# Kernel tuning notes

Measured on AMD Instinct MI355X. Metric: run time of the kernel, lower is better.

The kernel has to match this reference:

```python
import jax, jax.numpy as jnp
import numpy as np

B, C, H, W = 16, 128, 64, 64
NH = 8
HD = C // NH          # head dim == pos_embed_dim
WIN = 5               # relative-position window
OUT = 512             # out_dim of the final 1x1 projection


def _dwconv(x, w, pad):
    """Depthwise 2D conv, x: (N, Cin, H, W), w: (Cin, 1, kh, kw)."""
    return jax.lax.conv_general_dilated(
        x, w, window_strides=(1, 1), padding=[(pad, pad), (pad, pad)],
        dimension_numbers=('NCHW', 'OIHW', 'NCHW'),
        feature_group_count=x.shape[1])


def setup_inputs() -> dict:
    key = jax.random.key(0)
    ks = jax.random.split(key, 6)
    src = jax.random.normal(ks[0], (B, C, H, W), jnp.float32)
    cpe_w = jax.random.normal(ks[1], (C, 1, 3, 3), jnp.float32) * 0.1
    qkv_w = jax.random.normal(ks[2], (3 * C, C), jnp.float32) * (1.0 / np.sqrt(C))
    rel_pos = jax.random.normal(ks[3], (HD, WIN, WIN), jnp.float32) * 0.02
    conv1d_w = jax.random.normal(ks[4], (3,), jnp.float32) * 0.5
    out_w = jax.random.normal(ks[5], (OUT, 2 * C), jnp.float32) * (1.0 / np.sqrt(2 * C))
    return dict(src=src, cpe_w=cpe_w, qkv_w=qkv_w, rel_pos=rel_pos,
                conv1d_w=conv1d_w, out_w=out_w)


def reference(src, cpe_w, qkv_w, rel_pos, conv1d_w, out_w):
    scaling = HD ** (-0.5)
    feature_raw = src

    # CPE: depthwise 3x3 conv residual
    s = _dwconv(src, cpe_w, 1) + src

    # 1x1 QKV conv == channel GEMM
    qkv = jnp.einsum('oc,bchw->bohw', qkv_w, s)          # (B, 3C, H, W)
    q, k, v = jnp.split(qkv, 3, axis=1)                  # each (B, C, H, W)

    q = q.reshape(B * NH, HD, H, W)
    k = k.reshape(B * NH, HD, H, W)
    v = v.reshape(B * NH, HD, H, W)

    N = H * W
    kf = jax.nn.softmax(k.reshape(B * NH, HD, N), axis=-1)   # softmax over spatial
    vf = v.reshape(B * NH, HD, N)
    content_lambda = jnp.einsum('bin,bon->bio', kf, vf)      # (B*NH, HD, HD)
    qf = q.reshape(B * NH, HD, N) * scaling
    content_output = jnp.einsum('bin,bio->bon', qf, content_lambda)
    content_output = content_output.reshape(B * NH, HD, H, W)

    # relative-position lambda: depthwise 5x5 conv of v with rel_pos_embed
    position_lambda = _dwconv(v, rel_pos[:, None, :, :], WIN // 2)
    position_output = q * position_lambda

    result1 = (content_output + position_output).reshape(B, C, H, W)

    # ECA-style channel attention on the raw input
    pool = jnp.mean(feature_raw, axis=(2, 3))                # (B, C)
    xp = jnp.pad(pool, ((0, 0), (1, 1)))
    ca = jax.nn.sigmoid(conv1d_w[0] * xp[:, :-2]
                        + conv1d_w[1] * xp[:, 1:-1]
                        + conv1d_w[2] * xp[:, 2:])           # (B, C)
    result2 = feature_raw * ca[:, :, None, None]

    cat = jnp.concatenate([result1, result2], axis=1)       # (B, 2C, H, W)
    return jnp.einsum('oc,bchw->bohw', out_w, cat)           # (B, OUT, H, W)
```

## Files before the change

kernel.cpp:

```cpp
#include <hip/hip_runtime.h>
#include <hip/hip_bf16.h>
#include <math.h>

#define Bb   16
#define Cc   128
#define Hh   64
#define Wwid 64
#define Nn   4096
#define NHh  8
#define HDd  16
#define BHh  128
#define TCc  384
#define OUTc 512
#define KK2  256

typedef _Float16 f16x8 __attribute__((ext_vector_type(8)));
typedef float    f32x4 __attribute__((ext_vector_type(4)));

__device__ __forceinline__ ushort f2h_bits(float f) {
    _Float16 h = (_Float16)f;
    ushort u;
    __builtin_memcpy(&u, &h, 2);
    return u;
}
__device__ __forceinline__ float h2f_bits(ushort u) {
    _Float16 h;
    __builtin_memcpy(&h, &u, 2);
    return (float)h;
}

__global__ void cvt_weights(const float* __restrict__ a, int na,
                            const float* __restrict__ b2, int nb,
                            ushort* __restrict__ ya, ushort* __restrict__ yb) {
    int i = blockIdx.x * 256 + threadIdx.x;
    if (i < na) ya[i] = f2h_bits(a[i]);
    else if (i < na + nb) yb[i - na] = f2h_bits(b2[i - na]);
}

__global__ void __launch_bounds__(256) cpe_pool_kernel(const float* __restrict__ src,
                                                       const float* __restrict__ cpe_w,
                                                       ushort* __restrict__ s,
                                                       float* __restrict__ pool) {
    int bc = blockIdx.x;
    int c  = bc & (Cc - 1);
    const float* sp = src + (size_t)bc * Nn;
    __shared__ float pl[66 * 66];
    __shared__ float red[256];
    int t = threadIdx.x;
    for (int i = t; i < 66 * 66; i += 256) pl[i] = 0.f;
    __syncthreads();
    float lsum = 0.f;
    for (int i = t; i < Nn / 4; i += 256) {
        float4 v4 = ((const float4*)sp)[i];
        lsum += v4.x + v4.y + v4.z + v4.w;
        int e = i * 4, y = e >> 6, x = e & 63;
        float* d = &pl[(y + 1) * 66 + x + 1];
        d[0] = v4.x; d[1] = v4.y; d[2] = v4.z; d[3] = v4.w;
    }
    red[t] = lsum;
    float w[9];
#pragma unroll
    for (int k = 0; k < 9; k++) w[k] = cpe_w[c * 9 + k];
    __syncthreads();
    for (int s2 = 128; s2 > 0; s2 >>= 1) {
        if (t < s2) red[t] += red[t + s2];
        __syncthreads();
    }
    if (t == 0) pool[bc] = red[0] * (1.0f / Nn);
    int x = t & 63, ys = (t >> 6) * 16;
    float r[3][3];
#pragma unroll
    for (int k = 0; k < 2; k++)
#pragma unroll
        for (int j = 0; j < 3; j++) r[k][j] = pl[(ys + k) * 66 + x + j];
    ushort* dst = s + (size_t)bc * Nn;
#pragma unroll
    for (int yy = 0; yy < 16; yy++) {
        int y = ys + yy;
#pragma unroll
        for (int j = 0; j < 3; j++) r[2][j] = pl[(y + 2) * 66 + x + j];
        float acc = r[1][1];
#pragma unroll
        for (int k = 0; k < 3; k++)
#pragma unroll
            for (int j = 0; j < 3; j++) acc += r[k][j] * w[k * 3 + j];
        dst[y * 64 + x] = f2h_bits(acc);
#pragma unroll
        for (int j = 0; j < 3; j++) { r[0][j] = r[1][j]; r[1][j] = r[2][j]; }
    }
}

__global__ void ca_kernel(const float* __restrict__ pool,
                          const float* __restrict__ w3,
                          float* __restrict__ ca) {
    int i = blockIdx.x * 256 + threadIdx.x;
    if (i >= Bb * Cc) return;
    int c = i & (Cc - 1);
    float left  = (c == 0)        ? 0.f : pool[i - 1];
    float mid   = pool[i];
    float right = (c == Cc - 1)   ? 0.f : pool[i + 1];
    float v = w3[0] * left + w3[1] * mid + w3[2] * right;
    ca[i] = 1.f / (1.f + expf(-v));
}

__global__ void transpose_s(const ushort* __restrict__ s, ushort* __restrict__ sT) {
    int bz = blockIdx.z;
    int c0 = blockIdx.y * 64;
    int n0 = blockIdx.x * 64;
    __shared__ ushort t[64][68];
    int nn = threadIdx.x & 63, c4 = threadIdx.x >> 6;
    const ushort* sp = s + ((size_t)bz * Cc + c0) * Nn + n0;
#pragma unroll
    for (int p = 0; p < 16; p++) {
        int cc = p * 4 + c4;
        t[cc][nn] = sp[(size_t)cc * Nn + nn];
    }
    __syncthreads();
    int cw = threadIdx.x & 63, n4 = threadIdx.x >> 6;
    ushort* dp = sT + ((size_t)bz * Nn + n0) * Cc + c0;
#pragma unroll
    for (int p = 0; p < 16; p++) {
        int n = p * 4 + n4;
        dp[(size_t)n * Cc + cw] = t[cw][n];
    }
}

template<int K, int M, int MODE>
__global__ void __launch_bounds__(256) gemm_tn(const ushort* __restrict__ A,
                                               const ushort* __restrict__ Bt,
                                               float* __restrict__ C,
                                               ushort* __restrict__ q16,
                                               float* __restrict__ kf32,
                                               ushort* __restrict__ v16) {
    const int bz = blockIdx.z;
    const int m0 = blockIdx.y * 128;
    const int n0 = blockIdx.x * 128;
    __shared__ __align__(16) ushort Al[128 * 32];
    __shared__ __align__(16) ushort Bl[128 * 32];
    const int tid  = threadIdx.x;
    const int wave = tid >> 6, lane = tid & 63;
    const int r = lane & 15, q = lane >> 4;
    const int wr = wave >> 1, wc = wave & 1;

    const ushort* Ag = A + (size_t)m0 * K;
    const ushort* Bg = Bt + ((size_t)bz * Nn + n0) * K;

    f32x4 acc[4][4] = {};

    for (int k0 = 0; k0 < K; k0 += 32) {
#pragma unroll
        for (int p = 0; p < 2; p++) {
            int seg = p * 4 + wave;
            int idx = seg * 64 + lane;
            int row = idx >> 2, ch = idx & 3;
            const ushort* ga = Ag + (size_t)row * K + k0 + ch * 8;
            const ushort* gb = Bg + (size_t)row * K + k0 + ch * 8;
            __builtin_amdgcn_global_load_lds(
                (const __attribute__((address_space(1))) void*)(const void*)ga,
                (__attribute__((address_space(3))) void*)(void*)(Al + seg * 512),
                16, 0, 0);
            __builtin_amdgcn_global_load_lds(
                (const __attribute__((address_space(1))) void*)(const void*)gb,
                (__attribute__((address_space(3))) void*)(void*)(Bl + seg * 512),
                16, 0, 0);
        }
        __syncthreads();

        const ushort* Apt = Al + (size_t)(wr * 64 + r) * 32 + q * 8;
        const ushort* Bpt = Bl + (size_t)(wc * 64 + r) * 32 + q * 8;
        f16x8 af[4], bf[4];
#pragma unroll
        for (int i = 0; i < 4; i++) af[i] = *(const f16x8*)(Apt + i * 16 * 32);
#pragma unroll
        for (int j = 0; j < 4; j++) bf[j] = *(const f16x8*)(Bpt + j * 16 * 32);
#pragma unroll
        for (int i = 0; i < 4; i++)
#pragma unroll
            for (int j = 0; j < 4; j++)
                acc[i][j] = __builtin_amdgcn_mfma_f32_16x16x32_f16(af[i], bf[j], acc[i][j], 0, 0, 0);
        __syncthreads();
    }

    if constexpr (MODE == 0) {
        float* Cp = C + ((size_t)bz * M + m0 + wr * 64) * Nn + n0 + wc * 64;
#pragma unroll
        for (int i = 0; i < 4; i++)
#pragma unroll
            for (int j = 0; j < 4; j++)
#pragma unroll
                for (int e = 0; e < 4; e++)
                    Cp[(size_t)(i * 16 + q * 4 + e) * Nn + j * 16 + r] = acc[i][j][e];
    } else {
        size_t base = ((size_t)bz * Cc + wr * 64) * Nn + n0 + wc * 64;
        if (blockIdx.y == 1) {
            float* Cp = kf32 + base;
#pragma unroll
            for (int i = 0; i < 4; i++)
#pragma unroll
                for (int j = 0; j < 4; j++)
#pragma unroll
                    for (int e = 0; e < 4; e++)
                        Cp[(size_t)(i * 16 + q * 4 + e) * Nn + j * 16 + r] = acc[i][j][e];
        } else {
            ushort* Cp = (blockIdx.y == 0 ? q16 : v16) + base;
#pragma unroll
            for (int i = 0; i < 4; i++)
#pragma unroll
                for (int j = 0; j < 4; j++)
#pragma unroll
                    for (int e = 0; e < 4; e++)
                        Cp[(size_t)(i * 16 + q * 4 + e) * Nn + j * 16 + r] = f2h_bits(acc[i][j][e]);
        }
    }
}

__global__ void krowstat(const float* __restrict__ kf32,
                         float* __restrict__ mx, float* __restrict__ irs) {
    int row = blockIdx.x;
    const float* p = kf32 + (size_t)row * Nn;
    int t = threadIdx.x;
    __shared__ float red[256];
    float m = -1e30f;
    float vals[16];
#pragma unroll
    for (int j = 0; j < 16; j++) {
        vals[j] = p[t + j * 256];
        m = fmaxf(m, vals[j]);
    }
    red[t] = m; __syncthreads();
    for (int s2 = 128; s2 > 0; s2 >>= 1) {
        if (t < s2) red[t] = fmaxf(red[t], red[t + s2]);
        __syncthreads();
    }
    m = red[0]; __syncthreads();
    float sum = 0.f;
#pragma unroll
    for (int j = 0; j < 16; j++) sum += __expf(vals[j] - m);
    red[t] = sum; __syncthreads();
    for (int s2 = 128; s2 > 0; s2 >>= 1) {
        if (t < s2) red[t] += red[t + s2];
        __syncthreads();
    }
    if (t == 0) { mx[row] = m; irs[row] = 1.f / red[0]; }
}

__global__ void __launch_bounds__(256) lambda_mfma(const float* __restrict__ kf32,
                                                   const ushort* __restrict__ v16,
                                                   const float* __restrict__ mx,
                                                   const float* __restrict__ irs,
                                                   float* __restrict__ lamP) {
    int bh   = blockIdx.x >> 1;
    int half = blockIdx.x & 1;
    int b = bh >> 3, h = bh & 7;
    int wave = threadIdx.x >> 6, lane = threadIdx.x & 63;
    int r = lane & 15, q = lane >> 4;
    const float*  kf = kf32 + ((size_t)b * Cc + h * HDd) * Nn;
    const ushort* vf = v16  + ((size_t)b * Cc + h * HDd) * Nn;
    float mrow = mx[b * Cc + h * HDd + r];

    f32x4 acc = {};
    int nbase = half * 2048 + wave * 512;
#pragma unroll 4
    for (int s = 0; s < 16; s++) {
        int n = nbase + s * 32 + q * 8;
        float4 ka = *(const float4*)(kf + (size_t)r * Nn + n);
        float4 kb = *(const float4*)(kf + (size_t)r * Nn + n + 4);
        f16x8 bf = *(const f16x8*)(vf + (size_t)r * Nn + n);
        f16x8 af;
        af[0] = (_Float16)__expf(ka.x - mrow);
        af[1] = (_Float16)__expf(ka.y - mrow);
        af[2] = (_Float16)__expf(ka.z - mrow);
        af[3] = (_Float16)__expf(ka.w - mrow);
        af[4] = (_Float16)__expf(kb.x - mrow);
        af[5] = (_Float16)__expf(kb.y - mrow);
        af[6] = (_Float16)__expf(kb.z - mrow);
        af[7] = (_Float16)__expf(kb.w - mrow);
        acc = __builtin_amdgcn_mfma_f32_16x16x32_f16(af, bf, acc, 0, 0, 0);
    }

    __shared__ float red[4][256];
#pragma unroll
    for (int e = 0; e < 4; e++) red[wave][lane * 4 + e] = acc[e];
    __syncthreads();
    if (wave == 0) {
#pragma unroll
        for (int e = 0; e < 4; e++) {
            float v = red[0][lane * 4 + e] + red[1][lane * 4 + e]
                    + red[2][lane * 4 + e] + red[3][lane * 4 + e];
            int row = q * 4 + e;
            v *= irs[b * Cc + h * HDd + row];
            lamP[(size_t)half * (BHh * 256) + bh * 256 + row * 16 + r] = v;
        }
    }
}

__global__ void __launch_bounds__(256) poslam_kernel(const ushort* __restrict__ v16,
                                                     const float* __restrict__ rel,
                                                     ushort* __restrict__ pos) {
    int bc = blockIdx.x;
    int c = bc & (Cc - 1);
    const ushort* vp = v16 + (size_t)bc * Nn;
    __shared__ float pl[68 * 68];
    int t = threadIdx.x;
    for (int i = t; i < 68 * 68; i += 256) pl[i] = 0.f;
    __syncthreads();
    for (int i = t; i < Nn / 8; i += 256) {
        uint4 u = ((const uint4*)vp)[i];
        ushort us[8]; *(uint4*)us = u;
        int e = i * 8, y = e >> 6, x = e & 63;
        float* d = &pl[(y + 2) * 68 + x + 2];
#pragma unroll
        for (int j = 0; j < 8; j++) d[j] = h2f_bits(us[j]);
    }
    float w[25];
#pragma unroll
    for (int k = 0; k < 25; k++) w[k] = rel[(c & (HDd - 1)) * 25 + k];
    __syncthreads();
    int x = t & 63, ys = (t >> 6) * 16;
    float r[5][5];
#pragma unroll
    for (int k = 0; k < 4; k++)
#pragma unroll
        for (int j = 0; j < 5; j++) r[k][j] = pl[(ys + k) * 68 + x + j];
    ushort* dst = pos + (size_t)bc * Nn;
#pragma unroll
    for (int yy = 0; yy < 16; yy++) {
        int y = ys + yy;
#pragma unroll
        for (int j = 0; j < 5; j++) r[4][j] = pl[(y + 4) * 68 + x + j];
        float acc = 0.f;
#pragma unroll
        for (int k = 0; k < 5; k++)
#pragma unroll
            for (int j = 0; j < 5; j++) acc += r[k][j] * w[k * 5 + j];
        dst[y * 64 + x] = f2h_bits(acc);
#pragma unroll
        for (int k = 0; k < 4; k++)
#pragma unroll
            for (int j = 0; j < 5; j++) r[k][j] = r[k + 1][j];
    }
}

__global__ void combine_kernel(const ushort* __restrict__ q16,
                               const float* __restrict__ lamP,
                               const ushort* __restrict__ pos,
                               ushort* __restrict__ catT) {
    int bh   = blockIdx.x >> 4;
    int tile = blockIdx.x & 15;
    int n = tile * 256 + threadIdx.x;
    int b = bh >> 3, h = bh & 7;
    __shared__ float lam_s[256];
    lam_s[threadIdx.x] = lamP[bh * 256 + threadIdx.x]
                       + lamP[(size_t)(BHh * 256) + bh * 256 + threadIdx.x];
    __syncthreads();
    const ushort* qp = q16 + ((size_t)b * Cc + h * HDd) * Nn;
    float qv[16];
#pragma unroll
    for (int i = 0; i < 16; i++) qv[i] = h2f_bits(qp[(size_t)i * Nn + n]);
    const ushort* pp = pos + ((size_t)b * Cc + h * HDd) * Nn;
    float vals[16];
#pragma unroll
    for (int o = 0; o < 16; o++) {
        float co = 0.f;
#pragma unroll
        for (int i2 = 0; i2 < 16; i2++) co += qv[i2] * lam_s[i2 * 16 + o];
        vals[o] = co * 0.25f + qv[o] * h2f_bits(pp[(size_t)o * Nn + n]);
    }
    uint up[8];
#pragma unroll
    for (int o2 = 0; o2 < 8; o2++)
        up[o2] = (uint)f2h_bits(vals[2 * o2]) | ((uint)f2h_bits(vals[2 * o2 + 1]) << 16);
    uint4* dst = (uint4*)(catT + ((size_t)b * Nn + n) * KK2 + h * HDd);
    dst[0] = make_uint4(up[0], up[1], up[2], up[3]);
    dst[1] = make_uint4(up[4], up[5], up[6], up[7]);
}

__global__ void eca_cat(const float* __restrict__ src, const float* __restrict__ ca,
                        ushort* __restrict__ catT) {
    int bz = blockIdx.z, c0 = blockIdx.y * 64, n0 = blockIdx.x * 64;
    __shared__ ushort t[64][68];
    int nn = threadIdx.x & 63, c4 = threadIdx.x >> 6;
    const float* sp  = src + ((size_t)bz * Cc + c0) * Nn + n0;
    const float* cap = ca + bz * Cc + c0;
#pragma unroll
    for (int p = 0; p < 16; p++) {
        int cc = p * 4 + c4;
        t[cc][nn] = f2h_bits(sp[(size_t)cc * Nn + nn] * cap[cc]);
    }
    __syncthreads();
    int cw = threadIdx.x & 63, n4 = threadIdx.x >> 6;
    ushort* dp = catT + ((size_t)bz * Nn + n0) * KK2 + Cc + c0;
#pragma unroll
    for (int p = 0; p < 16; p++) {
        int n = p * 4 + n4;
        dp[(size_t)n * KK2 + cw] = t[cw][n];
    }
}

extern "C" void kernel_launch(void* const* d_in, const int* in_sizes, int n_in,
                              void* d_out, int out_size, void* d_ws, size_t ws_size,
                              hipStream_t stream) {
    const float* src      = (const float*)d_in[0];
    const float* cpe_w    = (const float*)d_in[1];
    const float* qkv_w    = (const float*)d_in[2];
    const float* rel_pos  = (const float*)d_in[3];
    const float* conv1d_w = (const float*)d_in[4];
    const float* out_w    = (const float*)d_in[5];
    float* out = (float*)d_out;

    char* ws = (char*)d_ws;
    ushort* q16   = (ushort*)ws;                                 ws += (size_t)Bb * Cc * Nn * 2;
    float*  kf32  = (float*)ws;                                  ws += (size_t)Bb * Cc * Nn * 4;
    ushort* v16   = (ushort*)ws;                                 ws += (size_t)Bb * Cc * Nn * 2;
    ushort* pos   = (ushort*)ws;                                 ws += (size_t)Bb * Cc * Nn * 2;
    ushort* catT  = (ushort*)ws;                                 ws += (size_t)Bb * Nn * KK2 * 2;
    ushort* sT    = (ushort*)ws;                                 ws += (size_t)Bb * Nn * Cc * 2;
    ushort* s16   = (ushort*)catT;
    float*  lamP  = (float*)ws;                                  ws += (size_t)2 * BHh * HDd * HDd * 4;
    float*  pool  = (float*)ws;                                  ws += Bb * Cc * 4;
    float*  ca    = (float*)ws;                                  ws += Bb * Cc * 4;
    float*  mx    = (float*)ws;                                  ws += Bb * Cc * 4;
    float*  irs   = (float*)ws;                                  ws += Bb * Cc * 4;
    ushort* wq16  = (ushort*)ws;                                 ws += (size_t)TCc * Cc * 2;
    ushort* wo16  = (ushort*)ws;                                 ws += (size_t)OUTc * KK2 * 2;

    {
        int na = TCc * Cc, nb = OUTc * KK2;
        cvt_weights<<<(na + nb + 255) / 256, 256, 0, stream>>>(qkv_w, na, out_w, nb, wq16, wo16);
    }
    cpe_pool_kernel<<<Bb * Cc, 256, 0, stream>>>(src, cpe_w, s16, pool);
    ca_kernel<<<(Bb * Cc + 255) / 256, 256, 0, stream>>>(pool, conv1d_w, ca);
    {
        dim3 g(Nn / 64, Cc / 64, Bb);
        transpose_s<<<g, 256, 0, stream>>>(s16, sT);
    }
    {
        dim3 g(Nn / 128, TCc / 128, Bb);
        gemm_tn<Cc, TCc, 1><<<g, 256, 0, stream>>>(wq16, sT, nullptr, q16, kf32, v16);
    }
    krowstat<<<Bb * Cc, 256, 0, stream>>>(kf32, mx, irs);
    lambda_mfma<<<2 * BHh, 256, 0, stream>>>(kf32, v16, mx, irs, lamP);
    poslam_kernel<<<Bb * Cc, 256, 0, stream>>>(v16, rel_pos, pos);
    combine_kernel<<<BHh * (Nn / 256), 256, 0, stream>>>(q16, lamP, pos, catT);
    {
        dim3 g(Nn / 64, Cc / 64, Bb);
        eca_cat<<<g, 256, 0, stream>>>(src, ca, catT);
    }
    {
        dim3 g(Nn / 128, OUTc / 128, Bb);
        gemm_tn<KK2, OUTc, 0><<<g, 256, 0, stream>>>(wo16, catT, out, nullptr, nullptr, nullptr);
    }
}
```

Before: 287.4 us.

## Merge independent kernels into combined launches and drop softmax max pass

```diff
diff --git a/kernel.cpp b/kernel.cpp
--- a/kernel.cpp
+++ b/kernel.cpp
@@ -29,24 +29,24 @@
     return (float)h;
 }
 
-__global__ void cvt_weights(const float* __restrict__ a, int na,
-                            const float* __restrict__ b2, int nb,
-                            ushort* __restrict__ ya, ushort* __restrict__ yb) {
-    int i = blockIdx.x * 256 + threadIdx.x;
-    if (i < na) ya[i] = f2h_bits(a[i]);
-    else if (i < na + nb) yb[i - na] = f2h_bits(b2[i - na]);
-}
-
-__global__ void __launch_bounds__(256) cpe_pool_kernel(const float* __restrict__ src,
-                                                       const float* __restrict__ cpe_w,
-                                                       ushort* __restrict__ s,
-                                                       float* __restrict__ pool) {
+__global__ void __launch_bounds__(256) cpe_cvt_kernel(
+        const float* __restrict__ src, const float* __restrict__ cpe_w,
+        const float* __restrict__ qkv_w, const float* __restrict__ out_w,
+        ushort* __restrict__ s, float* __restrict__ pool,
+        ushort* __restrict__ wq16, ushort* __restrict__ wo16) {
+    int t = threadIdx.x;
+    if (blockIdx.x >= 2048) {
+        int i = (blockIdx.x - 2048) * 256 + t;
+        const int na = TCc * Cc, nb = OUTc * KK2;
+        if (i < na) wq16[i] = f2h_bits(qkv_w[i]);
+        else if (i < na + nb) wo16[i - na] = f2h_bits(out_w[i - na]);
+        return;
+    }
     int bc = blockIdx.x;
     int c  = bc & (Cc - 1);
     const float* sp = src + (size_t)bc * Nn;
     __shared__ float pl[66 * 66];
     __shared__ float red[256];
-    int t = threadIdx.x;
     for (int i = t; i < 66 * 66; i += 256) pl[i] = 0.f;
     __syncthreads();
     float lsum = 0.f;
@@ -88,19 +88,6 @@
 #pragma unroll
         for (int j = 0; j < 3; j++) { r[0][j] = r[1][j]; r[1][j] = r[2][j]; }
     }
-}
-
-__global__ void ca_kernel(const float* __restrict__ pool,
-                          const float* __restrict__ w3,
-                          float* __restrict__ ca) {
-    int i = blockIdx.x * 256 + threadIdx.x;
-    if (i >= Bb * Cc) return;
-    int c = i & (Cc - 1);
-    float left  = (c == 0)        ? 0.f : pool[i - 1];
-    float mid   = pool[i];
-    float right = (c == Cc - 1)   ? 0.f : pool[i + 1];
-    float v = w3[0] * left + w3[1] * mid + w3[2] * right;
-    ca[i] = 1.f / (1.f + expf(-v));
 }
 
 __global__ void transpose_s(const ushort* __restrict__ s, ushort* __restrict__ sT) {
@@ -214,94 +201,75 @@
     }
 }
 
-__global__ void krowstat(const float* __restrict__ kf32,
-                         float* __restrict__ mx, float* __restrict__ irs) {
-    int row = blockIdx.x;
-    const float* p = kf32 + (size_t)row * Nn;
+__global__ void __launch_bounds__(256) lam_pos_kernel(
+        const float* __restrict__ kf32, const ushort* __restrict__ v16,
+        const float* __restrict__ rel,
+        ushort* __restrict__ pos, float* __restrict__ lamP,
+        float* __restrict__ lamE) {
+    __shared__ float smem[68 * 68];
     int t = threadIdx.x;
-    __shared__ float red[256];
-    float m = -1e30f;
-    float vals[16];
-#pragma unroll
-    for (int j = 0; j < 16; j++) {
-        vals[j] = p[t + j * 256];
-        m = fmaxf(m, vals[j]);
-    }
-    red[t] = m; __syncthreads();
-    for (int s2 = 128; s2 > 0; s2 >>= 1) {
-        if (t < s2) red[t] = fmaxf(red[t], red[t + s2]);
-        __syncthreads();
-    }
-    m = red[0]; __syncthreads();
-    float sum = 0.f;
-#pragma unroll
-    for (int j = 0; j < 16; j++) sum += __expf(vals[j] - m);
-    red[t] = sum; __syncthreads();
-    for (int s2 = 128; s2 > 0; s2 >>= 1) {
-        if (t < s2) red[t] += red[t + s2];
-        __syncthreads();
-    }
-    if (t == 0) { mx[row] = m; irs[row] = 1.f / red[0]; }
-}
-
-__global__ void __launch_bounds__(256) lambda_mfma(const float* __restrict__ kf32,
-                                                   const ushort* __restrict__ v16,
-                                                   const float* __restrict__ mx,
-                                                   const float* __restrict__ irs,
-                                                   float* __restrict__ lamP) {
-    int bh   = blockIdx.x >> 1;
-    int half = blockIdx.x & 1;
-    int b = bh >> 3, h = bh & 7;
-    int wave = threadIdx.x >> 6, lane = threadIdx.x & 63;
-    int r = lane & 15, q = lane >> 4;
-    const float*  kf = kf32 + ((size_t)b * Cc + h * HDd) * Nn;
-    const ushort* vf = v16  + ((size_t)b * Cc + h * HDd) * Nn;
-    float mrow = mx[b * Cc + h * HDd + r];
-
-    f32x4 acc = {};
-    int nbase = half * 2048 + wave * 512;
+
+    if (blockIdx.x >= 2048) {
+        int bid2 = blockIdx.x - 2048;
+        int bh   = bid2 >> 1;
+        int half = bid2 & 1;
+        int b = bh >> 3, h = bh & 7;
+        int wave = t >> 6, lane = t & 63;
+        int r = lane & 15, q = lane >> 4;
+        const float*  kf = kf32 + ((size_t)b * Cc + h * HDd) * Nn;
+        const ushort* vf = v16  + ((size_t)b * Cc + h * HDd) * Nn;
+
+        f32x4 acc = {};
+        float esum = 0.f;
+        int nbase = half * 2048 + wave * 512;
 #pragma unroll 4
-    for (int s = 0; s < 16; s++) {
-        int n = nbase + s * 32 + q * 8;
-        float4 ka = *(const float4*)(kf + (size_t)r * Nn + n);
-        float4 kb = *(const float4*)(kf + (size_t)r * Nn + n + 4);
-        f16x8 bf = *(const f16x8*)(vf + (size_t)r * Nn + n);
-        f16x8 af;
-        af[0] = (_Float16)__expf(ka.x - mrow);
-        af[1] = (_Float16)__expf(ka.y - mrow);
-        af[2] = (_Float16)__expf(ka.z - mrow);
-        af[3] = (_Float16)__expf(ka.w - mrow);
-        af[4] = (_Float16)__expf(kb.x - mrow);
-        af[5] = (_Float16)__expf(kb.y - mrow);
-        af[6] = (_Float16)__expf(kb.z - mrow);
-        af[7] = (_Float16)__expf(kb.w - mrow);
-        acc = __builtin_amdgcn_mfma_f32_16x16x32_f16(af, bf, acc, 0, 0, 0);
-    }
-
-    __shared__ float red[4][256];
-#pragma unroll
-    for (int e = 0; e < 4; e++) red[wave][lane * 4 + e] = acc[e];
-    __syncthreads();
-    if (wave == 0) {
-#pragma unroll
-        for (int e = 0; e < 4; e++) {
-            float v = red[0][lane * 4 + e] + red[1][lane * 4 + e]
-                    + red[2][lane * 4 + e] + red[3][lane * 4 + e];
-            int row = q * 4 + e;
-            v *= irs[b * Cc + h * HDd + row];
-            lamP[(size_t)half * (BHh * 256) + bh * 256 + row * 16 + r] = v;
-        }
-    }
-}
-
-__global__ void __launch_bounds__(256) poslam_kernel(const ushort* __restrict__ v16,
-                                                     const float* __restrict__ rel,
-                                                     ushort* __restrict__ pos) {
+        for (int s = 0; s < 16; s++) {
+            int n = nbase + s * 32 + q * 8;
+            float4 ka = *(const float4*)(kf + (size_t)r * Nn + n);
+            float4 kb = *(const float4*)(kf + (size_t)r * Nn + n + 4);
+            f16x8 bf = *(const f16x8*)(vf + (size_t)r * Nn + n);
+            float e0 = __expf(ka.x), e1 = __expf(ka.y), e2 = __expf(ka.z), e3 = __expf(ka.w);
+            float e4 = __expf(kb.x), e5 = __expf(kb.y), e6 = __expf(kb.z), e7 = __expf(kb.w);
+            esum += (e0 + e1 + e2 + e3) + (e4 + e5 + e6 + e7);
+            f16x8 af;
+            af[0] = (_Float16)e0; af[1] = (_Float16)e1;
+            af[2] = (_Float16)e2; af[3] = (_Float16)e3;
+            af[4] = (_Float16)e4; af[5] = (_Float16)e5;
+            af[6] = (_Float16)e6; af[7] = (_Float16)e7;
+            acc = __builtin_amdgcn_mfma_f32_16x16x32_f16(af, bf, acc, 0, 0, 0);
+        }
+
+        float* red   = smem;
+        float* esred = smem + 1024;
+#pragma unroll
+        for (int e = 0; e < 4; e++) red[wave * 256 + lane * 4 + e] = acc[e];
+        esred[wave * 64 + lane] = esum;
+        __syncthreads();
+        if (wave == 0) {
+#pragma unroll
+            for (int e = 0; e < 4; e++) {
+                float v = red[0 * 256 + lane * 4 + e] + red[1 * 256 + lane * 4 + e]
+                        + red[2 * 256 + lane * 4 + e] + red[3 * 256 + lane * 4 + e];
+                int row = q * 4 + e;
+                lamP[(size_t)half * (BHh * 256) + bh * 256 + row * 16 + r] = v;
+            }
+            if (lane < 16) {
+                float tot = 0.f;
+#pragma unroll
+                for (int w2 = 0; w2 < 4; w2++)
+#pragma unroll
+                    for (int qq = 0; qq < 4; qq++)
+                        tot += esred[w2 * 64 + qq * 16 + lane];
+                lamE[(size_t)half * (BHh * 16) + bh * 16 + lane] = tot;
+            }
+        }
+        return;
+    }
+
     int bc = blockIdx.x;
     int c = bc & (Cc - 1);
     const ushort* vp = v16 + (size_t)bc * Nn;
-    __shared__ float pl[68 * 68];
-    int t = threadIdx.x;
+    float* pl = smem;
     for (int i = t; i < 68 * 68; i += 256) pl[i] = 0.f;
     __syncthreads();
     for (int i = t; i < Nn / 8; i += 256) {
@@ -341,17 +309,57 @@
     }
 }
 
-__global__ void combine_kernel(const ushort* __restrict__ q16,
-                               const float* __restrict__ lamP,
-                               const ushort* __restrict__ pos,
-                               ushort* __restrict__ catT) {
+__global__ void __launch_bounds__(256) combine_eca_kernel(
+        const ushort* __restrict__ q16, const float* __restrict__ lamP,
+        const float* __restrict__ lamE, const ushort* __restrict__ pos,
+        const float* __restrict__ src, const float* __restrict__ pool,
+        const float* __restrict__ w3, ushort* __restrict__ catT) {
+    __shared__ float smem[2240];
+    int tid = threadIdx.x;
+
+    if (blockIdx.x >= 2048) {
+        int bid2 = blockIdx.x - 2048;
+        int n0 = (bid2 & 63) * 64, c0 = ((bid2 >> 6) & 1) * 64, bz = bid2 >> 7;
+        ushort* t = (ushort*)smem;
+        float* ca_s = smem + 2176;
+        if (tid < 64) {
+            int c = c0 + tid;
+            float left  = (c == 0)        ? 0.f : pool[bz * Cc + c - 1];
+            float mid   = pool[bz * Cc + c];
+            float right = (c == Cc - 1)   ? 0.f : pool[bz * Cc + c + 1];
+            float v = w3[0] * left + w3[1] * mid + w3[2] * right;
+            ca_s[tid] = 1.f / (1.f + __expf(-v));
+        }
+        __syncthreads();
+        int nn = tid & 63, c4 = tid >> 6;
+        const float* sp = src + ((size_t)bz * Cc + c0) * Nn + n0;
+#pragma unroll
+        for (int p = 0; p < 16; p++) {
+            int cc = p * 4 + c4;
+            t[cc * 68 + nn] = f2h_bits(sp[(size_t)cc * Nn + nn] * ca_s[cc]);
+        }
+        __syncthreads();
+        int cw = tid & 63, n4 = tid >> 6;
+        ushort* dp = catT + ((size_t)bz * Nn + n0) * KK2 + Cc + c0;
+#pragma unroll
+        for (int p = 0; p < 16; p++) {
+            int n = p * 4 + n4;
+            dp[(size_t)n * KK2 + cw] = t[cw * 68 + n];
+        }
+        return;
+    }
+
     int bh   = blockIdx.x >> 4;
     int tile = blockIdx.x & 15;
-    int n = tile * 256 + threadIdx.x;
+    int n = tile * 256 + tid;
     int b = bh >> 3, h = bh & 7;
-    __shared__ float lam_s[256];
-    lam_s[threadIdx.x] = lamP[bh * 256 + threadIdx.x]
-                       + lamP[(size_t)(BHh * 256) + bh * 256 + threadIdx.x];
+    float* lam_s = smem;
+    {
+        int i = tid >> 4;
+        float es = lamE[bh * 16 + i] + lamE[(size_t)(BHh * 16) + bh * 16 + i];
+        lam_s[tid] = (lamP[bh * 256 + tid]
+                    + lamP[(size_t)(BHh * 256) + bh * 256 + tid]) / es;
+    }
     __syncthreads();
     const ushort* qp = q16 + ((size_t)b * Cc + h * HDd) * Nn;
     float qv[16];
@@ -373,28 +381,6 @@
     uint4* dst = (uint4*)(catT + ((size_t)b * Nn + n) * KK2 + h * HDd);
     dst[0] = make_uint4(up[0], up[1], up[2], up[3]);
     dst[1] = make_uint4(up[4], up[5], up[6], up[7]);
-}
-
-__global__ void eca_cat(const float* __restrict__ src, const float* __restrict__ ca,
-                        ushort* __restrict__ catT) {
-    int bz = blockIdx.z, c0 = blockIdx.y * 64, n0 = blockIdx.x * 64;
-    __shared__ ushort t[64][68];
-    int nn = threadIdx.x & 63, c4 = threadIdx.x >> 6;
-    const float* sp  = src + ((size_t)bz * Cc + c0) * Nn + n0;
-    const float* cap = ca + bz * Cc + c0;
-#pragma unroll
-    for (int p = 0; p < 16; p++) {
-        int cc = p * 4 + c4;
-        t[cc][nn] = f2h_bits(sp[(size_t)cc * Nn + nn] * cap[cc]);
-    }
-    __syncthreads();
-    int cw = threadIdx.x & 63, n4 = threadIdx.x >> 6;
-    ushort* dp = catT + ((size_t)bz * Nn + n0) * KK2 + Cc + c0;
-#pragma unroll
-    for (int p = 0; p < 16; p++) {
-        int n = p * 4 + n4;
-        dp[(size_t)n * KK2 + cw] = t[cw][n];
-    }
 }
 
 extern "C" void kernel_launch(void* const* d_in, const int* in_sizes, int n_in,
@@ -416,20 +402,18 @@
     ushort* catT  = (ushort*)ws;                                 ws += (size_t)Bb * Nn * KK2 * 2;
     ushort* sT    = (ushort*)ws;                                 ws += (size_t)Bb * Nn * Cc * 2;
     ushort* s16   = (ushort*)catT;
-    float*  lamP  = (float*)ws;                                  ws += (size_t)2 * BHh * HDd * HDd * 4;
+    float*  lamP  = (float*)ws;                                  ws += (size_t)2 * BHh * 256 * 4;
+    float*  lamE  = (float*)ws;                                  ws += (size_t)2 * BHh * 16 * 4;
     float*  pool  = (float*)ws;                                  ws += Bb * Cc * 4;
-    float*  ca    = (float*)ws;                                  ws += Bb * Cc * 4;
-    float*  mx    = (float*)ws;                                  ws += Bb * Cc * 4;
-    float*  irs   = (float*)ws;                                  ws += Bb * Cc * 4;
     ushort* wq16  = (ushort*)ws;                                 ws += (size_t)TCc * Cc * 2;
     ushort* wo16  = (ushort*)ws;                                 ws += (size_t)OUTc * KK2 * 2;
 
     {
-        int na = TCc * Cc, nb = OUTc * KK2;
-        cvt_weights<<<(na + nb + 255) / 256, 256, 0, stream>>>(qkv_w, na, out_w, nb, wq16, wo16);
-    }
-    cpe_pool_kernel<<<Bb * Cc, 256, 0, stream>>>(src, cpe_w, s16, pool);
-    ca_kernel<<<(Bb * Cc + 255) / 256, 256, 0, stream>>>(pool, conv1d_w, ca);
+        const int nw = TCc * Cc + OUTc * KK2;
+        int cvt_blocks = (nw + 255) / 256;
+        cpe_cvt_kernel<<<2048 + cvt_blocks, 256, 0, stream>>>(
+            src, cpe_w, qkv_w, out_w, s16, pool, wq16, wo16);
+    }
     {
         dim3 g(Nn / 64, Cc / 64, Bb);
         transpose_s<<<g, 256, 0, stream>>>(s16, sT);
@@ -438,14 +422,9 @@
         dim3 g(Nn / 128, TCc / 128, Bb);
         gemm_tn<Cc, TCc, 1><<<g, 256, 0, stream>>>(wq16, sT, nullptr, q16, kf32, v16);
     }
-    krowstat<<<Bb * Cc, 256, 0, stream>>>(kf32, mx, irs);
-    lambda_mfma<<<2 * BHh, 256, 0, stream>>>(kf32, v16, mx, irs, lamP);
-    poslam_kernel<<<Bb * Cc, 256, 0, stream>>>(v16, rel_pos, pos);
-    combine_kernel<<<BHh * (Nn / 256), 256, 0, stream>>>(q16, lamP, pos, catT);
-    {
-        dim3 g(Nn / 64, Cc / 64, Bb);
-        eca_cat<<<g, 256, 0, stream>>>(src, ca, catT);
-    }
+    lam_pos_kernel<<<2048 + 2 * BHh, 256, 0, stream>>>(kf32, v16, rel_pos, pos, lamP, lamE);
+    combine_eca_kernel<<<2048 + 2048, 256, 0, stream>>>(
+        q16, lamP, lamE, pos, src, pool, conv1d_w, catT);
     {
         dim3 g(Nn / 128, OUTc / 128, Bb);
         gemm_tn<KK2, OUTc, 0><<<g, 256, 0, stream>>>(wo16, catT, out, nullptr, nullptr, nullptr);
```

Measured after the change: 268.3 us. 1.07x faster.
